# Kernel tuning notes

Hardware: AMD Instinct MI355X
Metric: run time of the kernel (lower is better)

## Reference

```python
import jax, jax.numpy as jnp
import numpy as np

H = 128
H1 = H + 1          # 129
FUSE = H1 * H1 * H1 # 2,146,689


def setup_inputs() -> dict:
    key = jax.random.key(0)
    ks = jax.random.split(key, 9)
    B = 64
    v = jax.random.normal(ks[0], (B, H), dtype=jnp.float32)
    a = jax.random.normal(ks[1], (B, H), dtype=jnp.float32)
    t = jax.random.normal(ks[2], (B, H), dtype=jnp.float32)
    # Linear params stored as [in, out]; xavier-ish scaling
    W1 = jax.random.normal(ks[3], (FUSE, H // 2), dtype=jnp.float32) * (1.0 / np.sqrt(FUSE))
    b1 = jnp.zeros((H // 2,), dtype=jnp.float32)
    W2 = jax.random.normal(ks[4], (H // 2, H // 4), dtype=jnp.float32) * (1.0 / np.sqrt(H // 2))
    b2 = jnp.zeros((H // 4,), dtype=jnp.float32)
    W3 = jax.random.normal(ks[5], (H // 4, 1), dtype=jnp.float32) * (1.0 / np.sqrt(H // 4))
    b3 = jnp.zeros((1,), dtype=jnp.float32)
    return {"v": v, "a": a, "t": t, "W1": W1, "b1": b1,
            "W2": W2, "b2": b2, "W3": W3, "b3": b3}


def reference(v, a, t, W1, b1, W2, b2, W3, b3):
    B = a.shape[0]
    one = jnp.ones((B, 1), dtype=a.dtype)
    a_h = jnp.concatenate([one, a], axis=1)  # [B, H+1]
    v_h = jnp.concatenate([one, v], axis=1)
    t_h = jnp.concatenate([one, t], axis=1)
    # triple outer product: fusion[b,i,j,k] = a_h[b,i]*v_h[b,j]*t_h[b,k]
    fusion = jnp.einsum('bi,bj,bk->bijk', a_h, v_h, t_h).reshape(B, -1)  # [B, (H+1)^3]
    # dropout p applied at eval is identity (torch Dropout in eval / p=0)
    y1 = jax.nn.relu(fusion @ W1 + b1)
    y2 = jax.nn.relu(y1 @ W2 + b2)
    return y2 @ W3 + b3  # [B, 1]
```

## Files before the change

### kernel.cpp

```cpp
#include <hip/hip_runtime.h>
#include <hip/hip_bf16.h>

#define H 128
#define H1 129
#define NSLAB (H1 * H1)
#define KP 164
#define NBLK 768
#define NREP 8

typedef __attribute__((ext_vector_type(8))) short short8;
typedef __attribute__((ext_vector_type(4))) float float4v;
typedef __attribute__((ext_vector_type(2))) int int2v;
typedef __attribute__((ext_vector_type(4))) int int4v;

__device__ __forceinline__ unsigned short f2bf_bits(float x) {
    return __builtin_bit_cast(unsigned short, __float2bfloat16(x));
}
__device__ __forceinline__ unsigned packbf(float x, float y) {
    return (unsigned)f2bf_bits(x) | ((unsigned)f2bf_bits(y) << 16);
}

__global__ __launch_bounds__(256, 3) void k1_partial(
        const float* __restrict__ v, const float* __restrict__ a,
        const float* __restrict__ t, const float* __restrict__ W1,
        float* __restrict__ acc)
{
    __shared__ short lds[64 * KP];

    const int tid  = threadIdx.x;
    const int wv   = tid >> 6;
    const int lane = tid & 63;
    const int quad = lane >> 4;
    const int l15  = lane & 15;

    for (int idx = tid; idx < 64 * (KP - 130); idx += 256) {
        int n = idx / (KP - 130), k = 130 + idx % (KP - 130);
        lds[n * KP + k] = 0;
    }

    short8 tf[5];
    const int bt = 16 * wv + l15;
    #pragma unroll
    for (int s = 0; s < 5; ++s) {
        #pragma unroll
        for (int j = 0; j < 8; ++j) {
            int k = 32 * s + 8 * quad + j;
            float val = (k == 0) ? 1.0f : ((k <= H) ? t[bt * H + k - 1] : 0.0f);
            tf[s][j] = (short)f2bf_bits(val);
        }
    }

    const float4v vz = {0.f, 0.f, 0.f, 0.f};
    float4v y1acc[4] = {vz, vz, vz, vz};

    const int s0 = (int)(((long long)blockIdx.x * NSLAB) / NBLK);
    const int s1 = (int)(((long long)(blockIdx.x + 1) * NSLAB) / NBLK);

    const int q = tid & 15;
    const int p16 = tid >> 4;
    const int br0 = 16 * wv + quad * 4;

    float4v ra[4], rb[4];
    float lastrow;
    float ahc[4], vhc[4], ahn[4], vhn[4];

    const float* Wb = W1 + (long long)s0 * (H1 * 64);

    auto ISSUE = [&](const float* Wp) {
        #pragma unroll
        for (int it = 0; it < 4; ++it) {
            int p = it * 16 + p16;
            ra[it] = *reinterpret_cast<const float4v*>(Wp + (2 * p) * 64 + q * 4);
            rb[it] = *reinterpret_cast<const float4v*>(Wp + (2 * p + 1) * 64 + q * 4);
        }
        lastrow = (tid < 64) ? Wp[128 * 64 + tid] : 0.f;
    };

    auto WRITE = [&]() {
        #pragma unroll
        for (int it = 0; it < 4; ++it) {
            int p = it * 16 + p16;
            #pragma unroll
            for (int c = 0; c < 4; ++c) {
                int n = q * 4 + c;
                *reinterpret_cast<unsigned*>(&lds[n * KP + 2 * p]) = packbf(ra[it][c], rb[it][c]);
            }
        }
        if (tid < 64)
            *reinterpret_cast<unsigned*>(&lds[tid * KP + 128]) = packbf(lastrow, 0.f);
    };

    auto LOADAV = [&](int si, int sj, float* ah, float* vh) {
        #pragma unroll
        for (int r = 0; r < 4; ++r) {
            int br = br0 + r;
            ah[r] = (si == 0) ? 1.0f : a[br * H + si - 1];
            vh[r] = (sj == 0) ? 1.0f : v[br * H + sj - 1];
        }
    };

    auto MFMA_ACC = [&]() {
        float4v D[4] = {vz, vz, vz, vz};
        #pragma unroll
        for (int s = 0; s < 5; ++s) {
            #pragma unroll
            for (int nt = 0; nt < 4; ++nt) {
                int n = nt * 16 + l15;
                int sa = n * KP + 32 * s + 8 * quad;
                int2v lo = *reinterpret_cast<const int2v*>(&lds[sa]);
                int2v hi = *reinterpret_cast<const int2v*>(&lds[sa + 4]);
                int4v w; w.x = lo.x; w.y = lo.y; w.z = hi.x; w.w = hi.y;
                short8 bf = __builtin_bit_cast(short8, w);
                D[nt] = __builtin_amdgcn_mfma_f32_16x16x32_bf16(tf[s], bf, D[nt], 0, 0, 0);
            }
        }
        float4v avv;
        #pragma unroll
        for (int r = 0; r < 4; ++r) avv[r] = ahc[r] * vhc[r];
        #pragma unroll
        for (int nt = 0; nt < 4; ++nt) y1acc[nt] += avv * D[nt];
    };

    int si = s0 / H1, sj = s0 % H1;
    ISSUE(Wb);
    LOADAV(si, sj, ahc, vhc);
    WRITE();
    Wb += H1 * 64;
    int si_n = si, sj_n = sj + 1; if (sj_n == H1) { sj_n = 0; ++si_n; }
    if (s0 + 1 < s1) { ISSUE(Wb); LOADAV(si_n, sj_n, ahn, vhn); }
    __syncthreads();

    for (int sl = s0 + 1; sl < s1; ++sl) {
        MFMA_ACC();
        #pragma unroll
        for (int r = 0; r < 4; ++r) { ahc[r] = ahn[r]; vhc[r] = vhn[r]; }
        __syncthreads();
        WRITE();
        Wb += H1 * 64;
        ++sj_n; if (sj_n == H1) { sj_n = 0; ++si_n; }
        if (sl + 1 < s1) { ISSUE(Wb); LOADAV(si_n, sj_n, ahn, vhn); }
        __syncthreads();
    }
    MFMA_ACC();

    const int rep = blockIdx.x & (NREP - 1);
    float* accr = acc + rep * (64 * 64);
    #pragma unroll
    for (int nt = 0; nt < 4; ++nt) {
        int h = nt * 16 + l15;
        #pragma unroll
        for (int r = 0; r < 4; ++r)
            unsafeAtomicAdd(&accr[(br0 + r) * 64 + h], y1acc[nt][r]);
    }
}

__global__ void k2_tail(const float* __restrict__ acc, const float* __restrict__ b1,
                        const float* __restrict__ W2, const float* __restrict__ b2,
                        const float* __restrict__ W3, const float* __restrict__ b3,
                        float* __restrict__ out)
{
    __shared__ float y1s[64 * 64];
    __shared__ float y2s[64 * 32];
    const int tid = threadIdx.x;

    for (int e = tid; e < 64 * 64; e += 256) {
        float x = b1[e & 63];
        #pragma unroll
        for (int r = 0; r < NREP; ++r) x += acc[r * 64 * 64 + e];
        y1s[e] = x > 0.f ? x : 0.f;
    }
    __syncthreads();
    for (int e = tid; e < 64 * 32; e += 256) {
        int b = e >> 5, h2 = e & 31;
        float s = b2[h2];
        #pragma unroll 8
        for (int h = 0; h < 64; ++h) s += y1s[b * 64 + h] * W2[h * 32 + h2];
        y2s[e] = s > 0.f ? s : 0.f;
    }
    __syncthreads();
    if (tid < 64) {
        float s = b3[0];
        #pragma unroll
        for (int h2 = 0; h2 < 32; ++h2) s += y2s[tid * 32 + h2] * W3[h2];
        out[tid] = s;
    }
}

extern "C" void kernel_launch(void* const* d_in, const int* in_sizes, int n_in,
                              void* d_out, int out_size, void* d_ws, size_t ws_size,
                              hipStream_t stream) {
    const float* v  = (const float*)d_in[0];
    const float* a  = (const float*)d_in[1];
    const float* t  = (const float*)d_in[2];
    const float* W1 = (const float*)d_in[3];
    const float* b1 = (const float*)d_in[4];
    const float* W2 = (const float*)d_in[5];
    const float* b2 = (const float*)d_in[6];
    const float* W3 = (const float*)d_in[7];
    const float* b3 = (const float*)d_in[8];
    float* acc = (float*)d_ws;

    hipMemsetAsync(acc, 0, NREP * 64 * 64 * sizeof(float), stream);
    hipLaunchKernelGGL(k1_partial, dim3(NBLK), dim3(256), 0, stream, v, a, t, W1, acc);
    hipLaunchKernelGGL(k2_tail, dim3(1), dim3(256), 0, stream,
                       acc, b1, W2, b2, W3, b3, (float*)d_out);
}
```

Before: 734.7 us.

## Load W1 fragments directly from global into MFMA operands, dropping LDS staging

Removes the shared-memory staging of each W1 slab, together with its double-buffered prefetch and the two barriers per slab. Each wave now reads W1 values straight from global memory in the MFMA B-fragment layout, converts them to bf16 in registers and issues the MFMAs. This is meant to cut LDS write/read traffic and synchronisation. In exchange, all four waves read the same W1 data redundantly using scalar strided loads, and there is no longer any explicit software prefetch to overlap memory latency with compute.

```diff
diff --git a/kernel.cpp b/kernel.cpp
--- a/kernel.cpp
+++ b/kernel.cpp
@@ -4,20 +4,14 @@
 #define H 128
 #define H1 129
 #define NSLAB (H1 * H1)
-#define KP 164
 #define NBLK 768
 #define NREP 8
 
 typedef __attribute__((ext_vector_type(8))) short short8;
 typedef __attribute__((ext_vector_type(4))) float float4v;
-typedef __attribute__((ext_vector_type(2))) int int2v;
-typedef __attribute__((ext_vector_type(4))) int int4v;
 
 __device__ __forceinline__ unsigned short f2bf_bits(float x) {
     return __builtin_bit_cast(unsigned short, __float2bfloat16(x));
-}
-__device__ __forceinline__ unsigned packbf(float x, float y) {
-    return (unsigned)f2bf_bits(x) | ((unsigned)f2bf_bits(y) << 16);
 }
 
 __global__ __launch_bounds__(256, 3) void k1_partial(
@@ -25,18 +19,11 @@
         const float* __restrict__ t, const float* __restrict__ W1,
         float* __restrict__ acc)
 {
-    __shared__ short lds[64 * KP];
-
     const int tid  = threadIdx.x;
     const int wv   = tid >> 6;
     const int lane = tid & 63;
     const int quad = lane >> 4;
     const int l15  = lane & 15;
-
-    for (int idx = tid; idx < 64 * (KP - 130); idx += 256) {
-        int n = idx / (KP - 130), k = 130 + idx % (KP - 130);
-        lds[n * KP + k] = 0;
-    }
 
     short8 tf[5];
     const int bt = 16 * wv + l15;
@@ -55,93 +42,52 @@
 
     const int s0 = (int)(((long long)blockIdx.x * NSLAB) / NBLK);
     const int s1 = (int)(((long long)(blockIdx.x + 1) * NSLAB) / NBLK);
-
-    const int q = tid & 15;
-    const int p16 = tid >> 4;
     const int br0 = 16 * wv + quad * 4;
 
-    float4v ra[4], rb[4];
-    float lastrow;
-    float ahc[4], vhc[4], ahn[4], vhn[4];
+    int si = s0 / H1, sj = s0 % H1;
+    const float* Wb = W1 + (long long)s0 * (H1 * 64);
+    const int lane_off = quad * (8 * 64) + l15;
 
-    const float* Wb = W1 + (long long)s0 * (H1 * 64);
-
-    auto ISSUE = [&](const float* Wp) {
-        #pragma unroll
-        for (int it = 0; it < 4; ++it) {
-            int p = it * 16 + p16;
-            ra[it] = *reinterpret_cast<const float4v*>(Wp + (2 * p) * 64 + q * 4);
-            rb[it] = *reinterpret_cast<const float4v*>(Wp + (2 * p + 1) * 64 + q * 4);
-        }
-        lastrow = (tid < 64) ? Wp[128 * 64 + tid] : 0.f;
-    };
-
-    auto WRITE = [&]() {
-        #pragma unroll
-        for (int it = 0; it < 4; ++it) {
-            int p = it * 16 + p16;
-            #pragma unroll
-            for (int c = 0; c < 4; ++c) {
-                int n = q * 4 + c;
-                *reinterpret_cast<unsigned*>(&lds[n * KP + 2 * p]) = packbf(ra[it][c], rb[it][c]);
-            }
-        }
-        if (tid < 64)
-            *reinterpret_cast<unsigned*>(&lds[tid * KP + 128]) = packbf(lastrow, 0.f);
-    };
-
-    auto LOADAV = [&](int si, int sj, float* ah, float* vh) {
+    for (int sl = s0; sl < s1; ++sl) {
+        float ah[4], vh[4];
         #pragma unroll
         for (int r = 0; r < 4; ++r) {
             int br = br0 + r;
             ah[r] = (si == 0) ? 1.0f : a[br * H + si - 1];
             vh[r] = (sj == 0) ? 1.0f : v[br * H + sj - 1];
         }
-    };
 
-    auto MFMA_ACC = [&]() {
         float4v D[4] = {vz, vz, vz, vz};
+        const float* Wl = Wb + lane_off;
         #pragma unroll
         for (int s = 0; s < 5; ++s) {
+            float wr[4][8];
             #pragma unroll
             for (int nt = 0; nt < 4; ++nt) {
-                int n = nt * 16 + l15;
-                int sa = n * KP + 32 * s + 8 * quad;
-                int2v lo = *reinterpret_cast<const int2v*>(&lds[sa]);
-                int2v hi = *reinterpret_cast<const int2v*>(&lds[sa + 4]);
-                int4v w; w.x = lo.x; w.y = lo.y; w.z = hi.x; w.w = hi.y;
-                short8 bf = __builtin_bit_cast(short8, w);
+                #pragma unroll
+                for (int j = 0; j < 8; ++j) {
+                    int kk = 32 * s + 8 * quad + j;
+                    wr[nt][j] = (kk <= H) ? Wl[(32 * s + j) * 64 + nt * 16] : 0.f;
+                }
+            }
+            #pragma unroll
+            for (int nt = 0; nt < 4; ++nt) {
+                short8 bf;
+                #pragma unroll
+                for (int j = 0; j < 8; ++j) bf[j] = (short)f2bf_bits(wr[nt][j]);
                 D[nt] = __builtin_amdgcn_mfma_f32_16x16x32_bf16(tf[s], bf, D[nt], 0, 0, 0);
             }
         }
+
         float4v avv;
         #pragma unroll
-        for (int r = 0; r < 4; ++r) avv[r] = ahc[r] * vhc[r];
+        for (int r = 0; r < 4; ++r) avv[r] = ah[r] * vh[r];
         #pragma unroll
         for (int nt = 0; nt < 4; ++nt) y1acc[nt] += avv * D[nt];
-    };
 
-    int si = s0 / H1, sj = s0 % H1;
-    ISSUE(Wb);
-    LOADAV(si, sj, ahc, vhc);
-    WRITE();
-    Wb += H1 * 64;
-    int si_n = si, sj_n = sj + 1; if (sj_n == H1) { sj_n = 0; ++si_n; }
-    if (s0 + 1 < s1) { ISSUE(Wb); LOADAV(si_n, sj_n, ahn, vhn); }
-    __syncthreads();
-
-    for (int sl = s0 + 1; sl < s1; ++sl) {
-        MFMA_ACC();
-        #pragma unroll
-        for (int r = 0; r < 4; ++r) { ahc[r] = ahn[r]; vhc[r] = vhn[r]; }
-        __syncthreads();
-        WRITE();
         Wb += H1 * 64;
-        ++sj_n; if (sj_n == H1) { sj_n = 0; ++si_n; }
-        if (sl + 1 < s1) { ISSUE(Wb); LOADAV(si_n, sj_n, ahn, vhn); }
-        __syncthreads();
+        ++sj; if (sj == H1) { sj = 0; ++si; }
     }
-    MFMA_ACC();
 
     const int rep = blockIdx.x & (NREP - 1);
     float* accr = acc + rep * (64 * 64);
```

After: 778.8 us. +6.0%, slower.
